# Kernel tuning notes

Hardware: AMD Instinct MI355X
Metric: run time of the kernel (lower is better)

The kernel has to match this reference:

```python
import jax, jax.numpy as jnp
import numpy as np

EPS = 1e-6
LN3 = 1.0986122886681098  # ternary_softmax uses base-3 exponentials: 3**x / sum(3**x)
ROPE_BASE = 10000.0


def exact_rmsnorm(x, g):
    # ExactRMSNorm: x / sqrt(mean(x^2) + eps) * g
    ms = jnp.mean(jnp.square(x), axis=-1, keepdims=True)
    return x * jax.lax.rsqrt(ms + EPS) * g


def ternary_rope(t):
    # Rotary embedding whose cos/sin tables are quantized to {-1, 0, +1}
    # (round() of cos/sin in [-1,1] yields exactly the ternary set).
    S, D = t.shape[-2], t.shape[-1]
    half = D // 2
    inv_freq = 1.0 / (ROPE_BASE ** (jnp.arange(half, dtype=jnp.float32) / half))
    ang = jnp.arange(S, dtype=jnp.float32)[:, None] * inv_freq[None, :]  # [S, half]
    cos = jnp.round(jnp.cos(ang))
    sin = jnp.round(jnp.sin(ang))
    cos = jnp.concatenate([cos, cos], axis=-1)  # [S, D]
    sin = jnp.concatenate([sin, sin], axis=-1)
    rot = jnp.concatenate([-t[..., half:], t[..., :half]], axis=-1)
    return t * cos + rot * sin


def ternary_softmax(x, axis=-1):
    # softmax in base 3: 3**x / sum(3**x) == softmax(x * ln 3)
    return jax.nn.softmax(x * LN3, axis=axis)


def setup_inputs() -> dict:
    key = jax.random.key(0)
    ks = jax.random.split(key, 6)
    B, S, D = 4, 4096, 1024
    x = jax.random.normal(ks[0], (B, S, D), dtype=jnp.float32)
    g_norm = jnp.ones((D,), dtype=jnp.float32)
    w_qkv = jax.random.normal(ks[1], (D, 3 * D), dtype=jnp.float32) * 0.02
    b_qkv = jnp.zeros((3 * D,), dtype=jnp.float32)
    w_proj = jax.random.normal(ks[2], (D, D), dtype=jnp.float32) * 0.02
    b_proj = jnp.zeros((D,), dtype=jnp.float32)
    return {"x": x, "g_norm": g_norm, "w_qkv": w_qkv, "b_qkv": b_qkv,
            "w_proj": w_proj, "b_proj": b_proj}


def reference(x, g_norm, w_qkv, b_qkv, w_proj, b_proj):
    D = x.shape[-1]
    scale = 1.0 / jnp.sqrt(jnp.float32(D))
    residual = x
    h = exact_rmsnorm(x, g_norm)
    qkv = h @ w_qkv + b_qkv  # [B, S, 3D]
    q, k, v = jnp.split(qkv, 3, axis=-1)
    q = ternary_rope(q)
    k = ternary_rope(k)
    scores = jnp.einsum("bsd,btd->bst", q, k) * scale  # [B, S, S]
    attn = ternary_softmax(scores, axis=-1)
    o = jnp.einsum("bst,btd->bsd", attn, v)
    return o @ w_proj + b_proj + residual
```

## Files before the change

kernel.cpp:

```cpp
#include <hip/hip_runtime.h>
#include <hip/hip_fp8.h>
#include <stdint.h>

#define DEVI __device__ __forceinline__

typedef unsigned short u16;
typedef uint8_t u8;
typedef __attribute__((ext_vector_type(8))) __bf16 bf16x8;
typedef __attribute__((ext_vector_type(4))) float f32x4;
typedef __attribute__((ext_vector_type(4))) int i32x4;
typedef __attribute__((ext_vector_type(8))) int i32x8;

DEVI float b2f(u16 u) { union { unsigned int i; float f; } v; v.i = ((unsigned int)u) << 16; return v.f; }
DEVI u16 f2b(float f) {
  union { float f; unsigned int i; } v; v.f = f;
  unsigned int r = v.i + 0x7fffu + ((v.i >> 16) & 1u);
  return (u16)(r >> 16);
}
DEVI u8 f2f8(float f) { __hip_fp8_e4m3 t(f); return t.__x; }

DEVI void gld_lds16(const void* g, void* l) {
  __builtin_amdgcn_global_load_lds((const __attribute__((address_space(1))) unsigned int*)g,
                                   (__attribute__((address_space(3))) unsigned int*)l, 16, 0, 0);
}

DEVI i32x8 ld32(const u8* p0, const u8* p1) {
  i32x4 lo = *(const i32x4*)p0;
  i32x4 hi = *(const i32x4*)p1;
  return __builtin_shufflevector(lo, hi, 0, 1, 2, 3, 4, 5, 6, 7);
}


__global__ __launch_bounds__(256) void k_rmsnorm(const float* __restrict__ x,
                                                 const float* __restrict__ g,
                                                 u8* __restrict__ h) {
  const int row = blockIdx.x;
  const int t = threadIdx.x;
  const float4 v = ((const float4*)(x + (size_t)row * 1024))[t];
  float ss = v.x * v.x + v.y * v.y + v.z * v.z + v.w * v.w;
  for (int off = 32; off > 0; off >>= 1) ss += __shfl_down(ss, off);
  __shared__ float red[4];
  if ((t & 63) == 0) red[t >> 6] = ss;
  __syncthreads();
  const float tot = red[0] + red[1] + red[2] + red[3];
  const float sc = rsqrtf(tot * (1.0f / 1024.0f) + 1e-6f);
  const float4 gv = ((const float4*)g)[t];
  uchar4 o;
  o.x = f2f8(v.x * sc * gv.x); o.y = f2f8(v.y * sc * gv.y);
  o.z = f2f8(v.z * sc * gv.z); o.w = f2f8(v.w * sc * gv.w);
  *(uchar4*)(h + (size_t)row * 1024 + t * 4) = o;
}

__global__ __launch_bounds__(256) void k_transpose_cast(const float* __restrict__ src,
                                                        int rows, int cols,
                                                        u16* __restrict__ dst) {
  __shared__ float tile[32][33];
  const int c0 = blockIdx.x * 32, r0 = blockIdx.y * 32;
  const int tx = threadIdx.x, ty = threadIdx.y;
  for (int i = 0; i < 32; i += 8)
    tile[ty + i][tx] = src[(size_t)(r0 + ty + i) * cols + c0 + tx];
  __syncthreads();
  for (int i = 0; i < 32; i += 8)
    dst[(size_t)(c0 + ty + i) * rows + r0 + tx] = f2b(tile[tx][ty + i]);
}

__global__ __launch_bounds__(256) void k_transpose_cast_f8(const float* __restrict__ src,
                                                           int rows, int cols,
                                                           u8* __restrict__ dst) {
  __shared__ float tile[32][33];
  const int c0 = blockIdx.x * 32, r0 = blockIdx.y * 32;
  const int tx = threadIdx.x, ty = threadIdx.y;
  for (int i = 0; i < 32; i += 8)
    tile[ty + i][tx] = src[(size_t)(r0 + ty + i) * cols + c0 + tx];
  __syncthreads();
  for (int i = 0; i < 32; i += 8)
    dst[(size_t)(c0 + ty + i) * rows + r0 + tx] = f2f8(tile[tx][ty + i] * 32.0f);
}

__global__ __launch_bounds__(256) void k_rope_cast(const u16* __restrict__ q16, const u16* __restrict__ k16,
                                                   u8* __restrict__ q8, u8* __restrict__ k8) {
  const int row = blockIdx.x;
  const int pos = row & 4095;
  const int t = threadIdx.x;
  const int j0 = t * 2;
  float c[2], s[2];
#pragma unroll
  for (int u = 0; u < 2; u++) {
    const float e = (float)(j0 + u) * (1.0f / 512.0f);
    const float invf = exp2f(-13.287712379549449f * e);
    const float ang = (float)pos * invf;
    c[u] = rintf(cosf(ang));
    s[u] = rintf(sinf(ang));
  }
  const u16* qr = q16 + (size_t)row * 1024;
  const u16* kr = k16 + (size_t)row * 1024;
  u8* qo = q8 + (size_t)row * 1024;
  u8* ko = k8 + (size_t)row * 1024;
  const ushort2 qa = *(const ushort2*)(qr + j0), qb = *(const ushort2*)(qr + j0 + 512);
  const ushort2 ka = *(const ushort2*)(kr + j0), kb = *(const ushort2*)(kr + j0 + 512);
  uchar2 o;
  o.x = f2f8(b2f(qa.x) * c[0] - b2f(qb.x) * s[0]);
  o.y = f2f8(b2f(qa.y) * c[1] - b2f(qb.y) * s[1]);
  *(uchar2*)(qo + j0) = o;
  o.x = f2f8(b2f(qb.x) * c[0] + b2f(qa.x) * s[0]);
  o.y = f2f8(b2f(qb.y) * c[1] + b2f(qa.y) * s[1]);
  *(uchar2*)(qo + j0 + 512) = o;
  o.x = f2f8(b2f(ka.x) * c[0] - b2f(kb.x) * s[0]);
  o.y = f2f8(b2f(ka.y) * c[1] - b2f(kb.y) * s[1]);
  *(uchar2*)(ko + j0) = o;
  o.x = f2f8(b2f(kb.x) * c[0] + b2f(ka.x) * s[0]);
  o.y = f2f8(b2f(kb.y) * c[1] + b2f(ka.y) * s[1]);
  *(uchar2*)(ko + j0 + 512) = o;
}

DEVI void gemm_tile(const u16* __restrict__ A, int lda,
                    const u16* __restrict__ B, int ldb,
                    int K, int m0, int n0,
                    u16* As, u16* Bs, f32x4 acc[4][4]) {
  const int t = threadIdx.x;
  const int sr = t >> 2;
  const int sc = (t & 3) * 8;
  const u16* Ag0 = A + (size_t)(m0 + sr) * lda + sc;
  const u16* Ag1 = A + (size_t)(m0 + 64 + sr) * lda + sc;
  const u16* Bg0 = B + (size_t)(n0 + sr) * ldb + sc;
  const u16* Bg1 = B + (size_t)(n0 + 64 + sr) * ldb + sc;
  u16* Asw = As + t * 8;
  u16* Bsw = Bs + t * 8;

  const int lane = t & 63, qd = lane >> 4, l16 = lane & 15;
  const int wave = t >> 6;
  const int wm = (wave >> 1) * 64, wn = (wave & 1) * 64;
  const int aoff = (wm + l16) * 32 + qd * 8;
  const int boff = (wn + l16) * 32 + qd * 8;

  auto stage = [&](int sel, int k0) {
    u16* Ad = Asw + sel * 4096;
    u16* Bd = Bsw + sel * 4096;
    gld_lds16(Ag0 + k0, Ad);
    gld_lds16(Ag1 + k0, Ad + 2048);
    gld_lds16(Bg0 + k0, Bd);
    gld_lds16(Bg1 + k0, Bd + 2048);
  };

  stage(0, 0);
  int cur = 0;
  for (int k0 = 0; k0 < K; k0 += 32) {
    if (k0 + 32 < K) {
      stage(cur ^ 1, k0 + 32);
      asm volatile("s_waitcnt vmcnt(4)" ::: "memory");
    } else {
      asm volatile("s_waitcnt vmcnt(0)" ::: "memory");
    }
    __builtin_amdgcn_s_barrier();
    const u16* Ard = As + cur * 4096 + aoff;
    const u16* Brd = Bs + cur * 4096 + boff;
    bf16x8 af[4], bfv[4];
#pragma unroll
    for (int i = 0; i < 4; i++) af[i] = *(const bf16x8*)(Ard + i * 16 * 32);
#pragma unroll
    for (int j = 0; j < 4; j++) bfv[j] = *(const bf16x8*)(Brd + j * 16 * 32);
    __builtin_amdgcn_s_setprio(1);
#pragma unroll
    for (int i = 0; i < 4; i++)
#pragma unroll
      for (int j = 0; j < 4; j++)
        acc[i][j] = __builtin_amdgcn_mfma_f32_16x16x32_bf16(af[i], bfv[j], acc[i][j], 0, 0, 0);
    __builtin_amdgcn_s_setprio(0);
    __builtin_amdgcn_s_barrier();
    cur ^= 1;
  }
}

DEVI void gemm_tile_mx2(const u8* __restrict__ A, int lda,
                        const u8* __restrict__ B, int ldb,
                        int K, int m0, int n0,
                        u8* As, u8* Bs, f32x4 acc[8][4], int sB) {
  const int t = threadIdx.x;
  const int sr = t >> 3;
  const int sc = ((t & 7) ^ (sr & 7)) << 4;
  const u8* Agb = A + (size_t)(m0 + sr) * lda + sc;
  const u8* Bgb = B + (size_t)(n0 + sr) * ldb + sc;
  u8* Asw = As + t * 16;
  u8* Bsw = Bs + t * 16;

  const int lane = t & 63, qd = lane >> 4, l16 = lane & 15;
  const int wave = t >> 6;
  const int wm = (wave >> 2) * 128, wn = (wave & 3) * 64;
  const int key = l16 & 7;
  const int c0 = ((qd << 1) ^ key) << 4;
  const int aoff = (wm + l16) * 128 + c0;
  const int boff = (wn + l16) * 128 + c0;

  auto stage = [&](int sel, int k0) {
    u8* Ad = Asw + sel * 32768;
    u8* Bd = Bsw + sel * 32768;
#pragma unroll
    for (int l = 0; l < 4; l++) {
      gld_lds16(Agb + k0 + (size_t)l * 64 * lda, Ad + l * 8192);
      gld_lds16(Bgb + k0 + (size_t)l * 64 * ldb, Bd + l * 8192);
    }
  };

  stage(0, 0);
  int cur = 0;
  for (int k0 = 0; k0 < K; k0 += 128) {
    if (k0 + 128 < K) {
      stage(cur ^ 1, k0 + 128);
      asm volatile("s_waitcnt vmcnt(8)" ::: "memory");
    } else {
      asm volatile("s_waitcnt vmcnt(0)" ::: "memory");
    }
    __builtin_amdgcn_s_barrier();
    const u8* Ab = As + cur * 32768;
    const u8* Bb = Bs + cur * 32768;
    i32x8 b[4];
#pragma unroll
    for (int j = 0; j < 4; j++)
      b[j] = ld32(Bb + boff + j * 2048, Bb + (boff ^ 16) + j * 2048);
#pragma unroll
    for (int i = 0; i < 8; i++) {
      const i32x8 a = ld32(Ab + aoff + i * 2048, Ab + (aoff ^ 16) + i * 2048);
      __builtin_amdgcn_s_setprio(1);
#pragma unroll
      for (int j = 0; j < 4; j++)
        acc[i][j] = __builtin_amdgcn_mfma_scale_f32_16x16x128_f8f6f4(
            a, b[j], acc[i][j], 0 , 0 ,
            0, 0x7f7f7f7f, 0, sB);
      __builtin_amdgcn_s_setprio(0);
    }
    __builtin_amdgcn_s_barrier();
    cur ^= 1;
  }
}

#define ACC_INIT4()                                              \
  f32x4 acc[4][4];                                               \
  _Pragma("unroll") for (int i = 0; i < 4; i++)                  \
      _Pragma("unroll") for (int j = 0; j < 4; j++)              \
          acc[i][j] = f32x4{0.f, 0.f, 0.f, 0.f};

#define ACC_INIT8()                                              \
  f32x4 acc[8][4];                                               \
  _Pragma("unroll") for (int i = 0; i < 8; i++)                  \
      _Pragma("unroll") for (int j = 0; j < 4; j++)              \
          acc[i][j] = f32x4{0.f, 0.f, 0.f, 0.f};

#define GEMM_EPI_IDX4()                                          \
  const int t = threadIdx.x, lane = t & 63, qd = lane >> 4,      \
            l16 = lane & 15, wave = t >> 6;                      \
  const int wm = (wave >> 1) * 64, wn = (wave & 1) * 64;         \
  (void)t;

#define GEMM_EPI_IDX8()                                          \
  const int t = threadIdx.x, lane = t & 63, qd = lane >> 4,      \
            l16 = lane & 15, wave = t >> 6;                      \
  const int wm = (wave >> 2) * 128, wn = (wave & 3) * 64;        \
  (void)t;


__global__ __launch_bounds__(512) void k_gemm_qkv(const u8* __restrict__ A, const u8* __restrict__ Bt,
                                                  const float* __restrict__ bias,
                                                  u16* __restrict__ q16, u16* __restrict__ k16,
                                                  u8* __restrict__ vt) {
  __shared__ alignas(16) u8 SMEM[131072];
  u8* As = SMEM;
  u8* Bs = SMEM + 65536;
  ACC_INIT8();
  const int m0 = blockIdx.y * 256, n0 = blockIdx.x * 256;
  gemm_tile_mx2(A, 1024, Bt, 1024, 1024, m0, n0, As, Bs, acc, 0x7a7a7a7a);
  GEMM_EPI_IDX8();
  const int sec = n0 >> 10;
  const int nb0 = n0 & 1023;
  if (sec < 2) {
    u16* dst = (sec == 0) ? q16 : k16;
#pragma unroll
    for (int i = 0; i < 8; i++) {
      const int mb = m0 + wm + i * 16 + qd * 4;
#pragma unroll
      for (int j = 0; j < 4; j++) {
        const int col = n0 + wn + j * 16 + l16;
        const float bv = bias[col];
        const int dcol = nb0 + wn + j * 16 + l16;
#pragma unroll
        for (int r = 0; r < 4; r++)
          dst[(size_t)(mb + r) * 1024 + dcol] = f2b(acc[i][j][r] + bv);
      }
    }
  } else {
    u8* T = SMEM;
    const int STR = 272;
#pragma unroll
    for (int i = 0; i < 8; i++) {
      const int mloc = wm + i * 16 + qd * 4;
#pragma unroll
      for (int j = 0; j < 4; j++) {
        const int dloc = wn + j * 16 + l16;
        const float bv = bias[n0 + wn + j * 16 + l16];
#pragma unroll
        for (int r = 0; r < 4; r++)
          T[dloc * STR + mloc + r] = f2f8(acc[i][j][r] + bv);
      }
    }
    __syncthreads();
    const int b = m0 >> 12;
    const int s0 = m0 & 4095;
    const int row = t >> 1, half = (t & 1) * 128;
    u8* dst = vt + ((size_t)(b * 1024 + nb0 + row)) * 4096 + s0 + half;
    const u8* src = T + row * STR + half;
#pragma unroll
    for (int c = 0; c < 8; c++)
      *(i32x4*)(dst + c * 16) = *(const i32x4*)(src + c * 16);
  }
}

__global__ __launch_bounds__(512) void k_gemm_scores(const u8* __restrict__ q, const u8* __restrict__ kk,
                                                     u8* __restrict__ P, float* __restrict__ ls) {
  __shared__ alignas(16) u8 SMEM[131072];
  u8* As = SMEM;
  u8* Bs = SMEM + 65536;
  ACC_INIT8();
  const int b = blockIdx.z;
  const u8* A = q + (size_t)b * 4096 * 1024;
  const u8* Bt = kk + (size_t)b * 4096 * 1024;
  const int bid = blockIdx.y * 16 + blockIdx.x;
  const int xcd = bid & 7, idx = bid >> 3;
  const int m0 = (idx & 15) * 256;
  const int n0 = ((xcd << 1) | (idx >> 4)) * 256;
  gemm_tile_mx2(A, 1024, Bt, 1024, 1024, m0, n0, As, Bs, acc, 0x7f7f7f7f);
  GEMM_EPI_IDX8();
  const float C3 = 0.04953007814753613f;
  const size_t Pb = (size_t)b * 4096 * 4096;
  f32x4 rowp[8];
#pragma unroll
  for (int i = 0; i < 8; i++) rowp[i] = f32x4{0.f, 0.f, 0.f, 0.f};
#pragma unroll
  for (int i = 0; i < 8; i++) {
    const int mb = m0 + wm + i * 16 + qd * 4;
#pragma unroll
    for (int j = 0; j < 4; j++) {
      const int col = n0 + wn + j * 16 + l16;
#pragma unroll
      for (int r = 0; r < 4; r++) {
        const float pv = __builtin_amdgcn_exp2f(acc[i][j][r] * C3);
        P[Pb + (size_t)(mb + r) * 4096 + col] = f2f8(pv);
        rowp[i][r] += pv;
      }
    }
  }
#pragma unroll
  for (int m = 1; m < 16; m <<= 1)
#pragma unroll
    for (int i = 0; i < 8; i++) {
      rowp[i].x += __shfl_xor(rowp[i].x, m);
      rowp[i].y += __shfl_xor(rowp[i].y, m);
      rowp[i].z += __shfl_xor(rowp[i].z, m);
      rowp[i].w += __shfl_xor(rowp[i].w, m);
    }
  if (l16 == 0) {
#pragma unroll
    for (int i = 0; i < 8; i++) {
      const int mb = m0 + wm + i * 16 + qd * 4;
#pragma unroll
      for (int r = 0; r < 4; r++)
        atomicAdd(ls + (size_t)b * 4096 + mb + r, rowp[i][r]);
    }
  }
}

__global__ __launch_bounds__(512) void k_gemm_pv(const u8* __restrict__ P, const u8* __restrict__ vt,
                                                 const float* __restrict__ ls, u16* __restrict__ o) {
  __shared__ alignas(16) u8 SMEM[131072];
  u8* As = SMEM;
  u8* Bs = SMEM + 65536;
  ACC_INIT8();
  const int b = blockIdx.z;
  const u8* A = P + (size_t)b * 4096 * 4096;
  const u8* Bt = vt + (size_t)b * 1024 * 4096;
  const int bid = blockIdx.y * 4 + blockIdx.x;
  const int xcd = bid & 7, idx = bid >> 3;
  const int m0 = (((xcd & 1) << 3) | idx) * 256;
  const int n0 = (xcd >> 1) * 256;
  gemm_tile_mx2(A, 4096, Bt, 4096, 4096, m0, n0, As, Bs, acc, 0x7f7f7f7f);
  GEMM_EPI_IDX8();
#pragma unroll
  for (int i = 0; i < 8; i++) {
    const int mb = m0 + wm + i * 16 + qd * 4;
    f32x4 inv;
#pragma unroll
    for (int r = 0; r < 4; r++) inv[r] = 1.0f / ls[(size_t)b * 4096 + mb + r];
#pragma unroll
    for (int j = 0; j < 4; j++) {
      const int col = n0 + wn + j * 16 + l16;
#pragma unroll
      for (int r = 0; r < 4; r++)
        o[(size_t)(b * 4096 + mb + r) * 1024 + col] = f2b(acc[i][j][r] * inv[r]);
    }
  }
}

__global__ __launch_bounds__(256) void k_gemm_proj(const u16* __restrict__ A, const u16* __restrict__ Bt,
                                                   const float* __restrict__ bias, const float* __restrict__ x,
                                                   float* __restrict__ out) {
  __shared__ alignas(16) u16 As[8192], Bs[8192];
  ACC_INIT4();
  const int m0 = blockIdx.y * 128, n0 = blockIdx.x * 128;
  gemm_tile(A, 1024, Bt, 1024, 1024, m0, n0, As, Bs, acc);
  GEMM_EPI_IDX4();
#pragma unroll
  for (int i = 0; i < 4; i++) {
    const int mb = m0 + wm + i * 16 + qd * 4;
#pragma unroll
    for (int j = 0; j < 4; j++) {
      const int col = n0 + wn + j * 16 + l16;
      const float bv = bias[col];
#pragma unroll
      for (int r = 0; r < 4; r++) {
        const size_t idxo = (size_t)(mb + r) * 1024 + col;
        out[idxo] = acc[i][j][r] + bv + x[idxo];
      }
    }
  }
}

extern "C" void kernel_launch(void* const* d_in, const int* in_sizes, int n_in,
                              void* d_out, int out_size, void* d_ws, size_t ws_size,
                              hipStream_t stream) {
  const float* x     = (const float*)d_in[0];
  const float* g     = (const float*)d_in[1];
  const float* wqkv  = (const float*)d_in[2];
  const float* bqkv  = (const float*)d_in[3];
  const float* wproj = (const float*)d_in[4];
  const float* bproj = (const float*)d_in[5];
  float* out = (float*)d_out;

  char* wsp = (char*)d_ws;
  size_t off = 0;
  auto take = [&](size_t bytes) -> void* {
    off = (off + 255) & ~(size_t)255;
    void* r = wsp + off;
    off += bytes;
    return r;
  };
  char* hreg = (char*)take(16384ull * 1024 * 2);
  u8*  h8   = (u8*)hreg;
  u16* o16  = (u16*)hreg;
  u8*  wqT8 = (u8*)take(3072ull * 1024);
  u16* wpT  = (u16*)take(1024ull * 1024 * 2);
  u8*  q8   = (u8*)take(16384ull * 1024);
  u8*  k8   = (u8*)take(16384ull * 1024);
  u8*  vt   = (u8*)take(4ull * 1024 * 4096);
  float* ls = (float*)take(16384ull * 4);
  char* scratch = (char*)take(3ull * 16384 * 1024 * 2);
  u16* q16 = (u16*)scratch;
  u16* k16 = (u16*)(scratch + 16384ull * 1024 * 2);
  u8*  P   = (u8*)scratch;

  k_transpose_cast_f8<<<dim3(3072 / 32, 1024 / 32), dim3(32, 8), 0, stream>>>(wqkv, 1024, 3072, wqT8);
  k_transpose_cast<<<dim3(1024 / 32, 1024 / 32), dim3(32, 8), 0, stream>>>(wproj, 1024, 1024, wpT);
  k_rmsnorm<<<16384, 256, 0, stream>>>(x, g, h8);
  k_gemm_qkv<<<dim3(12, 64), 512, 0, stream>>>(h8, wqT8, bqkv, q16, k16, vt);
  k_rope_cast<<<16384, 256, 0, stream>>>(q16, k16, q8, k8);
  hipMemsetAsync(ls, 0, 16384 * 4, stream);
  k_gemm_scores<<<dim3(16, 16, 4), 512, 0, stream>>>(q8, k8, P, ls);
  k_gemm_pv<<<dim3(4, 16, 4), 512, 0, stream>>>(P, vt, ls, o16);
  k_gemm_proj<<<dim3(8, 128), 256, 0, stream>>>(o16, wpT, bproj, x, out);
}
```

Measured before the change: 465.9 us.

## Interleave MX fp8 GEMM prefetch into four barrier-separated MFMA phases

Restructures the MX fp8 GEMM main loop so the next K-tile's global-to-LDS loads are issued inside the compute phases, with A loads in phase one and B loads in phase two, rather than all at the top of the iteration. Each iteration becomes four phases that each load two A fragments, sync with barriers and run eight scaled MFMAs. The aim is to spread memory issue across compute and keep waves in lockstep for better MFMA/LDS overlap. It adds barriers per iteration, which may cost stalls.

```diff
diff --git a/kernel.cpp b/kernel.cpp
--- a/kernel.cpp
+++ b/kernel.cpp
@@ -171,6 +171,25 @@
   }
 }
 
+#define MX_MFMA(IDX, AV)                                                     \
+  _Pragma("unroll") for (int j = 0; j < 4; j++)                              \
+      acc[IDX][j] = __builtin_amdgcn_mfma_scale_f32_16x16x128_f8f6f4(        \
+          AV, bfr[j], acc[IDX][j], 0, 0, 0, 0x7f7f7f7f, 0, sB);
+
+#define MX_PHASE(I0, I1, EXTRA)                                              \
+  {                                                                          \
+    i32x8 a0_ = ld32(Ab + aoff + (I0) * 2048, Ab + (aoff ^ 16) + (I0) * 2048); \
+    i32x8 a1_ = ld32(Ab + aoff + (I1) * 2048, Ab + (aoff ^ 16) + (I1) * 2048); \
+    EXTRA                                                                    \
+    __builtin_amdgcn_s_barrier();                                            \
+    asm volatile("s_waitcnt lgkmcnt(0)" ::: "memory");                       \
+    __builtin_amdgcn_s_setprio(1);                                           \
+    MX_MFMA(I0, a0_)                                                         \
+    MX_MFMA(I1, a1_)                                                         \
+    __builtin_amdgcn_s_setprio(0);                                           \
+    __builtin_amdgcn_s_barrier();                                            \
+  }
+
 DEVI void gemm_tile_mx2(const u8* __restrict__ A, int lda,
                         const u8* __restrict__ B, int ldb,
                         int K, int m0, int n0,
@@ -191,44 +210,45 @@
   const int aoff = (wm + l16) * 128 + c0;
   const int boff = (wn + l16) * 128 + c0;
 
-  auto stage = [&](int sel, int k0) {
-    u8* Ad = Asw + sel * 32768;
-    u8* Bd = Bsw + sel * 32768;
-#pragma unroll
-    for (int l = 0; l < 4; l++) {
-      gld_lds16(Agb + k0 + (size_t)l * 64 * lda, Ad + l * 8192);
-      gld_lds16(Bgb + k0 + (size_t)l * 64 * ldb, Bd + l * 8192);
-    }
-  };
-
-  stage(0, 0);
+#pragma unroll
+  for (int l = 0; l < 4; l++) {
+    gld_lds16(Agb + (size_t)l * 64 * lda, Asw + l * 8192);
+    gld_lds16(Bgb + (size_t)l * 64 * ldb, Bsw + l * 8192);
+  }
+  asm volatile("s_waitcnt vmcnt(0)" ::: "memory");
+  __builtin_amdgcn_s_barrier();
+
   int cur = 0;
   for (int k0 = 0; k0 < K; k0 += 128) {
-    if (k0 + 128 < K) {
-      stage(cur ^ 1, k0 + 128);
-      asm volatile("s_waitcnt vmcnt(8)" ::: "memory");
-    } else {
-      asm volatile("s_waitcnt vmcnt(0)" ::: "memory");
-    }
-    __builtin_amdgcn_s_barrier();
     const u8* Ab = As + cur * 32768;
     const u8* Bb = Bs + cur * 32768;
-    i32x8 b[4];
+    u8* Ad = Asw + (cur ^ 1) * 32768;
+    u8* Bd = Bsw + (cur ^ 1) * 32768;
+    const int kn = k0 + 128;
+    const bool more = kn < K;
+
+    i32x8 bfr[4];
 #pragma unroll
     for (int j = 0; j < 4; j++)
-      b[j] = ld32(Bb + boff + j * 2048, Bb + (boff ^ 16) + j * 2048);
-#pragma unroll
-    for (int i = 0; i < 8; i++) {
-      const i32x8 a = ld32(Ab + aoff + i * 2048, Ab + (aoff ^ 16) + i * 2048);
-      __builtin_amdgcn_s_setprio(1);
-#pragma unroll
-      for (int j = 0; j < 4; j++)
-        acc[i][j] = __builtin_amdgcn_mfma_scale_f32_16x16x128_f8f6f4(
-            a, b[j], acc[i][j], 0 , 0 ,
-            0, 0x7f7f7f7f, 0, sB);
-      __builtin_amdgcn_s_setprio(0);
-    }
-    __builtin_amdgcn_s_barrier();
+      bfr[j] = ld32(Bb + boff + j * 2048, Bb + (boff ^ 16) + j * 2048);
+
+    MX_PHASE(0, 1,
+      if (more) {
+        gld_lds16(Agb + kn, Ad);
+        gld_lds16(Agb + kn + (size_t)64 * lda, Ad + 8192);
+        gld_lds16(Agb + kn + (size_t)128 * lda, Ad + 16384);
+        gld_lds16(Agb + kn + (size_t)192 * lda, Ad + 24576);
+      })
+    MX_PHASE(2, 3,
+      if (more) {
+        gld_lds16(Bgb + kn, Bd);
+        gld_lds16(Bgb + kn + (size_t)64 * ldb, Bd + 8192);
+        gld_lds16(Bgb + kn + (size_t)128 * ldb, Bd + 16384);
+        gld_lds16(Bgb + kn + (size_t)192 * ldb, Bd + 24576);
+      })
+    MX_PHASE(4, 5, )
+    MX_PHASE(6, 7,
+      if (more) { asm volatile("s_waitcnt vmcnt(0)" ::: "memory"); })
     cur ^= 1;
   }
 }
```

Result: slower. 487.9 us (+4.7%).
